# Optimization experiments

Hardware: AMD Instinct MI355X
Metric: run time of the kernel (lower is better)

## Reference

```python
import jax, jax.numpy as jnp
import numpy as np

N_NODES = 100000
N_EDGES = 1000000
IN_FEATS = 128
HID = 128
OUT_FEATS = 64


def _glorot(key, shape):
    fan_in, fan_out = shape
    lim = (6.0 / (fan_in + fan_out)) ** 0.5
    return jax.random.uniform(key, shape, jnp.float32, -lim, lim)


def setup_inputs() -> dict:
    key = jax.random.key(0)
    ks = jax.random.split(key, 12)
    x = jax.random.normal(ks[0], (N_NODES, IN_FEATS), jnp.float32)
    src = jax.random.randint(ks[1], (N_EDGES,), 0, N_NODES, jnp.int32)
    dst = jax.random.randint(ks[2], (N_EDGES,), 0, N_NODES, jnp.int32)
    return {
        "x": x, "src": src, "dst": dst,
        "w_self0": _glorot(ks[3], (IN_FEATS, HID)),
        "w_neigh0": _glorot(ks[4], (IN_FEATS, HID)),
        "b0": jnp.zeros((HID,), jnp.float32),
        "w_self1": _glorot(ks[5], (HID, HID)),
        "w_neigh1": _glorot(ks[6], (HID, HID)),
        "b1": jnp.zeros((HID,), jnp.float32),
        "w_self2": _glorot(ks[7], (HID, OUT_FEATS)),
        "w_neigh2": _glorot(ks[8], (HID, OUT_FEATS)),
        "b2": jnp.zeros((OUT_FEATS,), jnp.float32),
    }


def _sage_conv(x, src, dst, deg_inv, w_self, w_neigh, b):
    # irregular gather over neighbors, then mean segment-reduce onto dst
    neigh_sum = jax.ops.segment_sum(x[src], dst, num_segments=x.shape[0])  # [N, d]
    neigh_mean = neigh_sum * deg_inv  # zero-in-degree nodes -> 0
    return x @ w_self + neigh_mean @ w_neigh + b


def reference(x, src, dst,
              w_self0, w_neigh0, b0,
              w_self1, w_neigh1, b1,
              w_self2, w_neigh2, b2):
    n = x.shape[0]
    deg = jax.ops.segment_sum(jnp.ones_like(dst, jnp.float32), dst, num_segments=n)
    deg_inv = jnp.where(deg > 0, 1.0 / jnp.maximum(deg, 1.0), 0.0)[:, None]  # [N,1]
    h = _sage_conv(x, src, dst, deg_inv, w_self0, w_neigh0, b0)
    h = jax.nn.relu(h)  # dropout is identity in eval
    h = _sage_conv(h, src, dst, deg_inv, w_self1, w_neigh1, b1)
    h = jax.nn.relu(h)
    h = _sage_conv(h, src, dst, deg_inv, w_self2, w_neigh2, b2)
    return h
```

## Files before the change

kernel.cpp:

```cpp
#include <hip/hip_runtime.h>
#include <stdint.h>

#define N_NODES 100000
#define N_EDGES 1000000
#define NB 782
#define CAP 4096
#define EPB 2048

typedef __attribute__((ext_vector_type(2))) _Float16 f16x2;
typedef __attribute__((ext_vector_type(8))) _Float16 f16x8;
typedef __attribute__((ext_vector_type(4))) float f32x4;

__device__ __forceinline__ unsigned short f2h(float f) {
  _Float16 h = (_Float16)f;
  return *(unsigned short*)&h;
}

__global__ void k_scatter(const int* __restrict__ src, const int* __restrict__ dst,
                          int* __restrict__ bcnt, unsigned int* __restrict__ stage) {
  __shared__ int h[NB];
  __shared__ int cur[NB];
  int t = threadIdx.x;
  for (int i = t; i < NB; i += 256) h[i] = 0;
  __syncthreads();
  int base = blockIdx.x * EPB;
#pragma unroll 8
  for (int k = 0; k < EPB / 256; k++) {
    int i = base + t + k * 256;
    if (i < N_EDGES) atomicAdd(&h[dst[i] >> 7], 1);
  }
  __syncthreads();
  for (int i = t; i < NB; i += 256) {
    int c = h[i];
    cur[i] = c ? atomicAdd(&bcnt[i], c) : 0;
  }
  __syncthreads();
#pragma unroll 8
  for (int k = 0; k < EPB / 256; k++) {
    int i = base + t + k * 256;
    if (i < N_EDGES) {
      int d = dst[i];
      int b = d >> 7;
      int pos = atomicAdd(&cur[b], 1);
      stage[(size_t)b * CAP + pos] = ((unsigned int)(d & 127) << 17) | (unsigned int)src[i];
    }
  }
}

__global__ __launch_bounds__(1024) void k_bscan(const int* __restrict__ bcnt,
                                                int* __restrict__ boff) {
  __shared__ int sc[1024];
  int t = threadIdx.x;
  int v = (t < NB) ? bcnt[t] : 0;
  sc[t] = v;
  __syncthreads();
  for (int off = 1; off < 1024; off <<= 1) {
    int a = (t >= off) ? sc[t - off] : 0;
    __syncthreads();
    sc[t] += a;
    __syncthreads();
  }
  if (t < NB) boff[t + 1] = sc[t];
  if (t == 0) boff[0] = 0;
}

__global__ void k_bucket(const unsigned int* __restrict__ stage, const int* __restrict__ boff,
                         int* __restrict__ csr, int* __restrict__ row_off,
                         float* __restrict__ dinv) {
  __shared__ int cnt[128], sc[128], cur[128];
  int b = blockIdx.x, t = threadIdx.x;
  int e0 = boff[b];
  int nb = boff[b + 1] - e0;
  const unsigned int* sb = stage + (size_t)b * CAP;
  if (t < 128) cnt[t] = 0;
  __syncthreads();
  for (int e = t; e < nb; e += 256)
    atomicAdd(&cnt[sb[e] >> 17], 1);
  __syncthreads();
  int myc = (t < 128) ? cnt[t] : 0;
  if (t < 128) sc[t] = myc;
  __syncthreads();
  for (int off = 1; off < 128; off <<= 1) {
    int a = (t < 128 && t >= off) ? sc[t - off] : 0;
    __syncthreads();
    if (t < 128) sc[t] += a;
    __syncthreads();
  }
  if (t < 128) {
    int node = b * 128 + t;
    int ex = sc[t] - myc;
    cur[t] = ex;
    if (node < N_NODES) {
      row_off[node] = e0 + ex;
      dinv[node] = myc ? 1.0f / (float)myc : 0.0f;
    }
  }
  if (b == NB - 1 && t == 0) row_off[N_NODES] = N_EDGES;
  __syncthreads();
  for (int e = t; e < nb; e += 256) {
    unsigned int v = sb[e];
    int l = v >> 17;
    int pos = e0 + atomicAdd(&cur[l], 1);
    csr[pos] = (int)(v & 0x1FFFFu);
  }
}

__global__ void k_prep(const float* __restrict__ x, unsigned short* __restrict__ xb,
                       const float* __restrict__ ws0, const float* __restrict__ wn0,
                       unsigned short* __restrict__ wt0,
                       const float* __restrict__ ws1, const float* __restrict__ wn1,
                       unsigned short* __restrict__ wt1,
                       const float* __restrict__ ws2, const float* __restrict__ wn2,
                       unsigned short* __restrict__ wt2) {
  int b = blockIdx.x;
  if (b < 6250) {
    int i = b * 256 + threadIdx.x;
    float4 a = ((const float4*)x)[2 * i];
    float4 v = ((const float4*)x)[2 * i + 1];
    unsigned short r[8] = {f2h(a.x), f2h(a.y), f2h(a.z), f2h(a.w),
                           f2h(v.x), f2h(v.y), f2h(v.z), f2h(v.w)};
    *(uint4*)(xb + (size_t)i * 8) = *(uint4*)r;
    return;
  }
  int t = (b - 6250) * 256 + threadIdx.x;
  const float* WS; const float* WN; unsigned short* WT; int nout;
  if (t < 16384) { WS = ws0; WN = wn0; WT = wt0; nout = 128; }
  else if (t < 32768) { t -= 16384; WS = ws1; WN = wn1; WT = wt1; nout = 128; }
  else { t -= 32768; if (t >= 8192) return; WS = ws2; WN = wn2; WT = wt2; nout = 64; }
  int n = t >> 7, k = t & 127;
  WT[n * 256 + k] = f2h(WS[(size_t)k * nout + n]);
  WT[n * 256 + 128 + k] = f2h(WN[(size_t)k * nout + n]);
}

__global__ void k_agg(const unsigned short* __restrict__ feat,
                      const int* __restrict__ row_off, const int* __restrict__ csr,
                      const float* __restrict__ dinv, unsigned short* __restrict__ nm) {
  int wv = threadIdx.x >> 6, lane = threadIdx.x & 63;
  int node = blockIdx.x * 4 + wv;
  if (node >= N_NODES) return;
  const uint4* fp = (const uint4*)feat;
  int s0 = row_off[node], s1 = row_off[node + 1];
  int g = lane >> 4, c = lane & 15;
  f16x2 q0 = {0, 0}, q1 = {0, 0}, q2 = {0, 0}, q3 = {0, 0};
  for (int j = s0 + g; j < s1; j += 16) {
    int i1 = j + 4, i2 = j + 8, i3 = j + 12;
    bool h1 = i1 < s1, h2 = i2 < s1, h3 = i3 < s1;
    int c0 = csr[j];
    int c1 = h1 ? csr[i1] : 0;
    int c2 = h2 ? csr[i2] : 0;
    int c3 = h3 ? csr[i3] : 0;
    uint4 v0, v1, v2, v3;
    v0 = fp[(size_t)c0 * 16 + c];
    if (h1) v1 = fp[(size_t)c1 * 16 + c];
    if (h2) v2 = fp[(size_t)c2 * 16 + c];
    if (h3) v3 = fp[(size_t)c3 * 16 + c];
    q0 += *(const f16x2*)&v0.x; q1 += *(const f16x2*)&v0.y;
    q2 += *(const f16x2*)&v0.z; q3 += *(const f16x2*)&v0.w;
    if (h1) {
      q0 += *(const f16x2*)&v1.x; q1 += *(const f16x2*)&v1.y;
      q2 += *(const f16x2*)&v1.z; q3 += *(const f16x2*)&v1.w;
    }
    if (h2) {
      q0 += *(const f16x2*)&v2.x; q1 += *(const f16x2*)&v2.y;
      q2 += *(const f16x2*)&v2.z; q3 += *(const f16x2*)&v2.w;
    }
    if (h3) {
      q0 += *(const f16x2*)&v3.x; q1 += *(const f16x2*)&v3.y;
      q2 += *(const f16x2*)&v3.z; q3 += *(const f16x2*)&v3.w;
    }
  }
  float a0 = (float)q0[0], a1 = (float)q0[1], a2 = (float)q1[0], a3 = (float)q1[1];
  float a4 = (float)q2[0], a5 = (float)q2[1], a6 = (float)q3[0], a7 = (float)q3[1];
#define RED(x) x += __shfl_xor(x, 16); x += __shfl_xor(x, 32);
  RED(a0) RED(a1) RED(a2) RED(a3) RED(a4) RED(a5) RED(a6) RED(a7)
#undef RED
  if (g == 0) {
    float di = dinv[node];
    uint4 o;
    o.x = ((unsigned int)f2h(a1 * di) << 16) | (unsigned int)f2h(a0 * di);
    o.y = ((unsigned int)f2h(a3 * di) << 16) | (unsigned int)f2h(a2 * di);
    o.z = ((unsigned int)f2h(a5 * di) << 16) | (unsigned int)f2h(a4 * di);
    o.w = ((unsigned int)f2h(a7 * di) << 16) | (unsigned int)f2h(a6 * di);
    ((uint4*)(nm + (size_t)node * 128))[c] = o;
  }
}

template <int NOUT, bool RELU, bool OUT_F16>
__global__ __launch_bounds__(256, 4) void k_mm(
    const unsigned short* __restrict__ A0, const unsigned short* __restrict__ A1,
    const unsigned short* __restrict__ WT, const float* __restrict__ Bv,
    void* __restrict__ OUT) {
  constexpr int NFC = NOUT / 64;
  __shared__ __align__(16) unsigned short sm[16896];
  const int row0 = blockIdx.x * 64;
  const int tid = threadIdx.x;

  for (int i = tid; i < 1024; i += 256) {
    int r = i >> 4, c = i & 15;
    int gr = row0 + r;
    if (gr >= N_NODES) gr = N_NODES - 1;
    *(uint4*)(sm + r * 264 + c * 8) = ((const uint4*)(A0 + (size_t)gr * 128))[c];
    *(uint4*)(sm + r * 264 + 128 + c * 8) = ((const uint4*)(A1 + (size_t)gr * 128))[c];
  }

  const int lane = tid & 63;
  const int w = tid >> 6;
  const int r16 = lane & 15;
  const int kg = lane >> 4;
  const int wc0 = w * (NOUT / 4);

  f32x4 acc[4][NFC];
#pragma unroll
  for (int rf = 0; rf < 4; rf++)
#pragma unroll
    for (int cf = 0; cf < NFC; cf++) acc[rf][cf] = (f32x4){0.f, 0.f, 0.f, 0.f};

  __syncthreads();

  const unsigned short* wtb = WT + (size_t)(wc0 + r16) * 256 + kg * 8;
  const unsigned short* asb = sm + r16 * 264 + kg * 8;

  for (int ks = 0; ks < 8; ks++) {
    f16x8 a[4];
#pragma unroll
    for (int rf = 0; rf < 4; rf++)
      a[rf] = *(const f16x8*)(asb + rf * 16 * 264 + ks * 32);
#pragma unroll
    for (int cf = 0; cf < NFC; cf++) {
      f16x8 b = *(const f16x8*)(wtb + cf * 16 * 256 + ks * 32);
#pragma unroll
      for (int rf = 0; rf < 4; rf++)
        acc[rf][cf] = __builtin_amdgcn_mfma_f32_16x16x32_f16(a[rf], b, acc[rf][cf], 0, 0, 0);
    }
  }

  __syncthreads();

  if (OUT_F16) {
    constexpr int LSO = NOUT + 8;
    unsigned short* so = sm;
#pragma unroll
    for (int rf = 0; rf < 4; rf++)
#pragma unroll
      for (int cf = 0; cf < NFC; cf++) {
        int col = wc0 + cf * 16 + r16;
        float bias = Bv[col];
#pragma unroll
        for (int r = 0; r < 4; r++) {
          int row = rf * 16 + kg * 4 + r;
          float v = acc[rf][cf][r] + bias;
          if (RELU) v = fmaxf(v, 0.f);
          so[row * LSO + col] = f2h(v);
        }
      }
    __syncthreads();
    unsigned short* O = (unsigned short*)OUT;
    for (int i = tid; i < 64 * (NOUT / 8); i += 256) {
      int r = i / (NOUT / 8), c = i % (NOUT / 8);
      int gr = row0 + r;
      if (gr < N_NODES)
        *(uint4*)(O + (size_t)gr * NOUT + c * 8) = *(const uint4*)(so + r * LSO + c * 8);
    }
  } else {
    constexpr int LSO = NOUT + 4;
    float* so = (float*)sm;
#pragma unroll
    for (int rf = 0; rf < 4; rf++)
#pragma unroll
      for (int cf = 0; cf < NFC; cf++) {
        int col = wc0 + cf * 16 + r16;
        float bias = Bv[col];
#pragma unroll
        for (int r = 0; r < 4; r++) {
          int row = rf * 16 + kg * 4 + r;
          float v = acc[rf][cf][r] + bias;
          if (RELU) v = fmaxf(v, 0.f);
          so[row * LSO + col] = v;
        }
      }
    __syncthreads();
    float* O = (float*)OUT;
    for (int i = tid; i < 64 * (NOUT / 4); i += 256) {
      int r = i / (NOUT / 4), c = i % (NOUT / 4);
      int gr = row0 + r;
      if (gr < N_NODES)
        *(float4*)(O + (size_t)gr * NOUT + c * 4) = *(const float4*)(so + r * LSO + c * 4);
    }
  }
}


extern "C" void kernel_launch(void* const* d_in, const int* in_sizes, int n_in,
                              void* d_out, int out_size, void* d_ws, size_t ws_size,
                              hipStream_t stream) {
  const float* x   = (const float*)d_in[0];
  const int*   src = (const int*)d_in[1];
  const int*   dst = (const int*)d_in[2];
  const float* ws0 = (const float*)d_in[3];
  const float* wn0 = (const float*)d_in[4];
  const float* b0  = (const float*)d_in[5];
  const float* ws1 = (const float*)d_in[6];
  const float* wn1 = (const float*)d_in[7];
  const float* b1  = (const float*)d_in[8];
  const float* ws2 = (const float*)d_in[9];
  const float* wn2 = (const float*)d_in[10];
  const float* b2  = (const float*)d_in[11];
  float* out = (float*)d_out;

  uint8_t* base = (uint8_t*)d_ws;
  size_t off = 0;
  auto alloc = [&](size_t bytes) -> void* {
    void* p = base + off;
    off = (off + bytes + 255) & ~(size_t)255;
    return p;
  };
  int*   row_off = (int*)alloc((size_t)(N_NODES + 1) * 4);
  float* dinv    = (float*)alloc((size_t)N_NODES * 4);
  int*   csr     = (int*)alloc((size_t)N_EDGES * 4);
  unsigned int* stage = (unsigned int*)alloc((size_t)NB * CAP * 4);
  int*   bcnt    = (int*)alloc((size_t)NB * 4);
  int*   boff    = (int*)alloc((size_t)(NB + 1) * 4);
  unsigned short* xb  = (unsigned short*)alloc((size_t)N_NODES * 128 * 2);
  unsigned short* nmb = (unsigned short*)alloc((size_t)N_NODES * 128 * 2);
  unsigned short* h1b = (unsigned short*)alloc((size_t)N_NODES * 128 * 2);
  unsigned short* h2b = (unsigned short*)alloc((size_t)N_NODES * 128 * 2);
  unsigned short* wt0 = (unsigned short*)alloc(128 * 256 * 2);
  unsigned short* wt1 = (unsigned short*)alloc(128 * 256 * 2);
  unsigned short* wt2 = (unsigned short*)alloc(64 * 256 * 2);

  hipMemsetAsync(bcnt, 0, (size_t)NB * 4, stream);
  k_scatter<<<(N_EDGES + EPB - 1) / EPB, 256, 0, stream>>>(src, dst, bcnt, stage);
  k_bscan<<<1, 1024, 0, stream>>>(bcnt, boff);
  k_bucket<<<NB, 256, 0, stream>>>(stage, boff, csr, row_off, dinv);

  k_prep<<<6410, 256, 0, stream>>>(x, xb, ws0, wn0, wt0, ws1, wn1, wt1, ws2, wn2, wt2);

  const int GMM = (N_NODES + 63) / 64;

  k_agg<<<25000, 256, 0, stream>>>(xb, row_off, csr, dinv, nmb);
  k_mm<128, true, true><<<GMM, 256, 0, stream>>>(xb, nmb, wt0, b0, h1b);
  k_agg<<<25000, 256, 0, stream>>>(h1b, row_off, csr, dinv, nmb);
  k_mm<128, true, true><<<GMM, 256, 0, stream>>>(h1b, nmb, wt1, b1, h2b);
  k_agg<<<25000, 256, 0, stream>>>(h2b, row_off, csr, dinv, nmb);
  k_mm<64, false, false><<<GMM, 256, 0, stream>>>(h2b, nmb, wt2, b2, out);
}
```

Baseline: 255.7 us.

## Fuse scatter with prep kernel and drop bucket prefix scan via padded CSR

Merges the edge scatter and the fp16 conversion/weight transpose into one launch, with block ranges choosing the role. It removes the single-block bucket scan by giving each bucket a fixed CAP-sized region of the CSR array and storing separate row begin and end arrays. This saves two kernel launches and one serial scan, at the cost of a larger, padded CSR buffer and an extra index array read in each aggregation.

```diff
diff --git a/kernel.cpp b/kernel.cpp
--- a/kernel.cpp
+++ b/kernel.cpp
@@ -6,6 +6,8 @@
 #define NB 782
 #define CAP 4096
 #define EPB 2048
+#define SCB ((N_EDGES + EPB - 1) / EPB)
+#define PREPB 6410
 
 typedef __attribute__((ext_vector_type(2))) _Float16 f16x2;
 typedef __attribute__((ext_vector_type(8))) _Float16 f16x8;
@@ -16,105 +18,48 @@
   return *(unsigned short*)&h;
 }
 
-__global__ void k_scatter(const int* __restrict__ src, const int* __restrict__ dst,
-                          int* __restrict__ bcnt, unsigned int* __restrict__ stage) {
+__global__ void k_scatter_prep(const int* __restrict__ src, const int* __restrict__ dst,
+                               int* __restrict__ bcnt, unsigned int* __restrict__ stage,
+                               const float* __restrict__ x, unsigned short* __restrict__ xb,
+                               const float* __restrict__ ws0, const float* __restrict__ wn0,
+                               unsigned short* __restrict__ wt0,
+                               const float* __restrict__ ws1, const float* __restrict__ wn1,
+                               unsigned short* __restrict__ wt1,
+                               const float* __restrict__ ws2, const float* __restrict__ wn2,
+                               unsigned short* __restrict__ wt2) {
   __shared__ int h[NB];
   __shared__ int cur[NB];
   int t = threadIdx.x;
-  for (int i = t; i < NB; i += 256) h[i] = 0;
-  __syncthreads();
-  int base = blockIdx.x * EPB;
+  if (blockIdx.x < SCB) {
+    for (int i = t; i < NB; i += 256) h[i] = 0;
+    __syncthreads();
+    int base = blockIdx.x * EPB;
 #pragma unroll 8
-  for (int k = 0; k < EPB / 256; k++) {
-    int i = base + t + k * 256;
-    if (i < N_EDGES) atomicAdd(&h[dst[i] >> 7], 1);
-  }
-  __syncthreads();
-  for (int i = t; i < NB; i += 256) {
-    int c = h[i];
-    cur[i] = c ? atomicAdd(&bcnt[i], c) : 0;
-  }
-  __syncthreads();
+    for (int k = 0; k < EPB / 256; k++) {
+      int i = base + t + k * 256;
+      if (i < N_EDGES) atomicAdd(&h[dst[i] >> 7], 1);
+    }
+    __syncthreads();
+    for (int i = t; i < NB; i += 256) {
+      int c = h[i];
+      cur[i] = c ? atomicAdd(&bcnt[i], c) : 0;
+    }
+    __syncthreads();
 #pragma unroll 8
-  for (int k = 0; k < EPB / 256; k++) {
-    int i = base + t + k * 256;
-    if (i < N_EDGES) {
-      int d = dst[i];
-      int b = d >> 7;
-      int pos = atomicAdd(&cur[b], 1);
-      stage[(size_t)b * CAP + pos] = ((unsigned int)(d & 127) << 17) | (unsigned int)src[i];
-    }
-  }
-}
-
-__global__ __launch_bounds__(1024) void k_bscan(const int* __restrict__ bcnt,
-                                                int* __restrict__ boff) {
-  __shared__ int sc[1024];
-  int t = threadIdx.x;
-  int v = (t < NB) ? bcnt[t] : 0;
-  sc[t] = v;
-  __syncthreads();
-  for (int off = 1; off < 1024; off <<= 1) {
-    int a = (t >= off) ? sc[t - off] : 0;
-    __syncthreads();
-    sc[t] += a;
-    __syncthreads();
-  }
-  if (t < NB) boff[t + 1] = sc[t];
-  if (t == 0) boff[0] = 0;
-}
-
-__global__ void k_bucket(const unsigned int* __restrict__ stage, const int* __restrict__ boff,
-                         int* __restrict__ csr, int* __restrict__ row_off,
-                         float* __restrict__ dinv) {
-  __shared__ int cnt[128], sc[128], cur[128];
-  int b = blockIdx.x, t = threadIdx.x;
-  int e0 = boff[b];
-  int nb = boff[b + 1] - e0;
-  const unsigned int* sb = stage + (size_t)b * CAP;
-  if (t < 128) cnt[t] = 0;
-  __syncthreads();
-  for (int e = t; e < nb; e += 256)
-    atomicAdd(&cnt[sb[e] >> 17], 1);
-  __syncthreads();
-  int myc = (t < 128) ? cnt[t] : 0;
-  if (t < 128) sc[t] = myc;
-  __syncthreads();
-  for (int off = 1; off < 128; off <<= 1) {
-    int a = (t < 128 && t >= off) ? sc[t - off] : 0;
-    __syncthreads();
-    if (t < 128) sc[t] += a;
-    __syncthreads();
-  }
-  if (t < 128) {
-    int node = b * 128 + t;
-    int ex = sc[t] - myc;
-    cur[t] = ex;
-    if (node < N_NODES) {
-      row_off[node] = e0 + ex;
-      dinv[node] = myc ? 1.0f / (float)myc : 0.0f;
-    }
-  }
-  if (b == NB - 1 && t == 0) row_off[N_NODES] = N_EDGES;
-  __syncthreads();
-  for (int e = t; e < nb; e += 256) {
-    unsigned int v = sb[e];
-    int l = v >> 17;
-    int pos = e0 + atomicAdd(&cur[l], 1);
-    csr[pos] = (int)(v & 0x1FFFFu);
-  }
-}
-
-__global__ void k_prep(const float* __restrict__ x, unsigned short* __restrict__ xb,
-                       const float* __restrict__ ws0, const float* __restrict__ wn0,
-                       unsigned short* __restrict__ wt0,
-                       const float* __restrict__ ws1, const float* __restrict__ wn1,
-                       unsigned short* __restrict__ wt1,
-                       const float* __restrict__ ws2, const float* __restrict__ wn2,
-                       unsigned short* __restrict__ wt2) {
-  int b = blockIdx.x;
+    for (int k = 0; k < EPB / 256; k++) {
+      int i = base + t + k * 256;
+      if (i < N_EDGES) {
+        int d = dst[i];
+        int b = d >> 7;
+        int pos = atomicAdd(&cur[b], 1);
+        stage[(size_t)b * CAP + pos] = ((unsigned int)(d & 127) << 17) | (unsigned int)src[i];
+      }
+    }
+    return;
+  }
+  int b = blockIdx.x - SCB;
   if (b < 6250) {
-    int i = b * 256 + threadIdx.x;
+    int i = b * 256 + t;
     float4 a = ((const float4*)x)[2 * i];
     float4 v = ((const float4*)x)[2 * i + 1];
     unsigned short r[8] = {f2h(a.x), f2h(a.y), f2h(a.z), f2h(a.w),
@@ -122,24 +67,66 @@
     *(uint4*)(xb + (size_t)i * 8) = *(uint4*)r;
     return;
   }
-  int t = (b - 6250) * 256 + threadIdx.x;
+  int w = (b - 6250) * 256 + t;
   const float* WS; const float* WN; unsigned short* WT; int nout;
-  if (t < 16384) { WS = ws0; WN = wn0; WT = wt0; nout = 128; }
-  else if (t < 32768) { t -= 16384; WS = ws1; WN = wn1; WT = wt1; nout = 128; }
-  else { t -= 32768; if (t >= 8192) return; WS = ws2; WN = wn2; WT = wt2; nout = 64; }
-  int n = t >> 7, k = t & 127;
+  if (w < 16384) { WS = ws0; WN = wn0; WT = wt0; nout = 128; }
+  else if (w < 32768) { w -= 16384; WS = ws1; WN = wn1; WT = wt1; nout = 128; }
+  else { w -= 32768; if (w >= 8192) return; WS = ws2; WN = wn2; WT = wt2; nout = 64; }
+  int n = w >> 7, k = w & 127;
   WT[n * 256 + k] = f2h(WS[(size_t)k * nout + n]);
   WT[n * 256 + 128 + k] = f2h(WN[(size_t)k * nout + n]);
 }
 
+__global__ void k_bucket(const unsigned int* __restrict__ stage, const int* __restrict__ bcnt,
+                         int* __restrict__ csr, int* __restrict__ rowbeg,
+                         int* __restrict__ rowend, float* __restrict__ dinv) {
+  __shared__ int cnt[128], sc[128], cur[128];
+  int b = blockIdx.x, t = threadIdx.x;
+  int nb = bcnt[b];
+  const unsigned int* sb = stage + (size_t)b * CAP;
+  int e0 = b * CAP;
+  if (t < 128) cnt[t] = 0;
+  __syncthreads();
+  for (int e = t; e < nb; e += 256)
+    atomicAdd(&cnt[sb[e] >> 17], 1);
+  __syncthreads();
+  int myc = (t < 128) ? cnt[t] : 0;
+  if (t < 128) sc[t] = myc;
+  __syncthreads();
+  for (int off = 1; off < 128; off <<= 1) {
+    int a = (t < 128 && t >= off) ? sc[t - off] : 0;
+    __syncthreads();
+    if (t < 128) sc[t] += a;
+    __syncthreads();
+  }
+  if (t < 128) {
+    int node = b * 128 + t;
+    int ex = sc[t] - myc;
+    cur[t] = ex;
+    if (node < N_NODES) {
+      rowbeg[node] = e0 + ex;
+      rowend[node] = e0 + ex + myc;
+      dinv[node] = myc ? 1.0f / (float)myc : 0.0f;
+    }
+  }
+  __syncthreads();
+  for (int e = t; e < nb; e += 256) {
+    unsigned int v = sb[e];
+    int l = v >> 17;
+    int pos = e0 + atomicAdd(&cur[l], 1);
+    csr[pos] = (int)(v & 0x1FFFFu);
+  }
+}
+
 __global__ void k_agg(const unsigned short* __restrict__ feat,
-                      const int* __restrict__ row_off, const int* __restrict__ csr,
+                      const int* __restrict__ rowbeg, const int* __restrict__ rowend,
+                      const int* __restrict__ csr,
                       const float* __restrict__ dinv, unsigned short* __restrict__ nm) {
   int wv = threadIdx.x >> 6, lane = threadIdx.x & 63;
   int node = blockIdx.x * 4 + wv;
   if (node >= N_NODES) return;
   const uint4* fp = (const uint4*)feat;
-  int s0 = row_off[node], s1 = row_off[node + 1];
+  int s0 = rowbeg[node], s1 = rowend[node];
   int g = lane >> 4, c = lane & 15;
   f16x2 q0 = {0, 0}, q1 = {0, 0}, q2 = {0, 0}, q3 = {0, 0};
   for (int j = s0 + g; j < s1; j += 16) {
@@ -314,12 +301,12 @@
     off = (off + bytes + 255) & ~(size_t)255;
     return p;
   };
-  int*   row_off = (int*)alloc((size_t)(N_NODES + 1) * 4);
+  int*   rowbeg  = (int*)alloc((size_t)N_NODES * 4);
+  int*   rowend  = (int*)alloc((size_t)N_NODES * 4);
   float* dinv    = (float*)alloc((size_t)N_NODES * 4);
-  int*   csr     = (int*)alloc((size_t)N_EDGES * 4);
+  int*   csr     = (int*)alloc((size_t)NB * CAP * 4);
   unsigned int* stage = (unsigned int*)alloc((size_t)NB * CAP * 4);
   int*   bcnt    = (int*)alloc((size_t)NB * 4);
-  int*   boff    = (int*)alloc((size_t)(NB + 1) * 4);
   unsigned short* xb  = (unsigned short*)alloc((size_t)N_NODES * 128 * 2);
   unsigned short* nmb = (unsigned short*)alloc((size_t)N_NODES * 128 * 2);
   unsigned short* h1b = (unsigned short*)alloc((size_t)N_NODES * 128 * 2);
@@ -329,18 +316,17 @@
   unsigned short* wt2 = (unsigned short*)alloc(64 * 256 * 2);
 
   hipMemsetAsync(bcnt, 0, (size_t)NB * 4, stream);
-  k_scatter<<<(N_EDGES + EPB - 1) / EPB, 256, 0, stream>>>(src, dst, bcnt, stage);
-  k_bscan<<<1, 1024, 0, stream>>>(bcnt, boff);
-  k_bucket<<<NB, 256, 0, stream>>>(stage, boff, csr, row_off, dinv);
-
-  k_prep<<<6410, 256, 0, stream>>>(x, xb, ws0, wn0, wt0, ws1, wn1, wt1, ws2, wn2, wt2);
+  k_scatter_prep<<<SCB + PREPB, 256, 0, stream>>>(src, dst, bcnt, stage,
+                                                  x, xb, ws0, wn0, wt0,
+                                                  ws1, wn1, wt1, ws2, wn2, wt2);
+  k_bucket<<<NB, 256, 0, stream>>>(stage, bcnt, csr, rowbeg, rowend, dinv);
 
   const int GMM = (N_NODES + 63) / 64;
 
-  k_agg<<<25000, 256, 0, stream>>>(xb, row_off, csr, dinv, nmb);
+  k_agg<<<25000, 256, 0, stream>>>(xb, rowbeg, rowend, csr, dinv, nmb);
   k_mm<128, true, true><<<GMM, 256, 0, stream>>>(xb, nmb, wt0, b0, h1b);
-  k_agg<<<25000, 256, 0, stream>>>(h1b, row_off, csr, dinv, nmb);
+  k_agg<<<25000, 256, 0, stream>>>(h1b, rowbeg, rowend, csr, dinv, nmb);
   k_mm<128, true, true><<<GMM, 256, 0, stream>>>(h1b, nmb, wt1, b1, h2b);
-  k_agg<<<25000, 256, 0, stream>>>(h2b, row_off, csr, dinv, nmb);
+  k_agg<<<25000, 256, 0, stream>>>(h2b, rowbeg, rowend, csr, dinv, nmb);
   k_mm<64, false, false><<<GMM, 256, 0, stream>>>(h2b, nmb, wt2, b2, out);
 }
```

Result: faster. 246.9 us (-3.4%).
